# Kernel tuning notes

Measured on AMD Instinct MI355X. Metric: run time of the kernel, lower is better.

Reference implementation:

```python
import jax, jax.numpy as jnp
import numpy as np

B, X, H = 2048, 1024, 1024
DR = 0.5

def setup_inputs() -> dict:
    key = jax.random.key(0)
    ks = jax.random.split(key, 21)
    std = 1.0 / np.sqrt(H)
    u = lambda k, s: jax.random.uniform(k, s, jnp.float32, -std, std)
    bern = lambda k, s: (jax.random.bernoulli(k, 1.0 - DR, s) / (1.0 - DR)).astype(jnp.float32)
    return {
        "x": jax.random.normal(ks[0], (B, X), jnp.float32),
        "h0": jax.random.normal(ks[1], (B, H), jnp.float32),
        "c0": jax.random.normal(ks[2], (B, H), jnp.float32),
        "w_xi": u(ks[3], (H, X)), "w_xf": u(ks[4], (H, X)),
        "w_xc": u(ks[5], (H, X)), "w_xo": u(ks[6], (H, X)),
        "w_hi": u(ks[7], (H, H)), "w_hf": u(ks[8], (H, H)),
        "w_hc": u(ks[9], (H, H)), "w_ho": u(ks[10], (H, H)),
        "b_i": u(ks[11], (H,)), "b_f": u(ks[12], (H,)),
        "b_c": u(ks[13], (H,)), "b_o": u(ks[14], (H,)),
        "maskHI": bern(ks[15], (B, H)), "maskHF": bern(ks[16], (B, H)),
        "maskHC": bern(ks[17], (B, H)), "maskHO": bern(ks[18], (B, H)),
        "maskC": bern(ks[19], (B, H)),
    }

def reference(x, h0, c0,
              w_xi, w_xf, w_xc, w_xo,
              w_hi, w_hf, w_hc, w_ho,
              b_i, b_f, b_c, b_o,
              maskHI, maskHF, maskHC, maskHO, maskC):
    # gal dropout: per-gate masks on recurrent input h0
    hs = jnp.stack([h0 * maskHI, h0 * maskHF, h0 * maskHC, h0 * maskHO])  # [4,B,H]
    wh = jnp.stack([w_hi, w_hf, w_hc, w_ho])                              # [4,H,H]
    wx = jnp.stack([w_xi, w_xf, w_xc, w_xo])                              # [4,H,X]
    # two batched GEMMs (F.linear uses x @ W.T)
    g = jnp.einsum('bx,gkx->gbk', x, wx) + jnp.einsum('gbh,gkh->gbk', hs, wh)
    gateI = jax.nn.sigmoid(g[0] + b_i)
    gateF = jax.nn.sigmoid(g[1] + b_f)
    gateC = jnp.tanh(g[2] + b_c) * maskC   # sem dropout on candidate
    gateO = jax.nn.sigmoid(g[3] + b_o)
    c1 = gateF * c0 + gateI * gateC
    h1 = gateO * jnp.tanh(c1)
    return (h1, c1)
```

## Files before the change

### kernel.cpp

```cpp
#include <hip/hip_runtime.h>
#include <hip/hip_bf16.h>
#include <stdint.h>

#define BDIM 2048
#define HDIM 1024
#define XDIM 1024
#define BH (BDIM*HDIM)
#define WSEG 1048576

typedef __attribute__((ext_vector_type(8))) short short8;
typedef __attribute__((ext_vector_type(4))) float float4v;

__device__ __forceinline__ void gload16(const void* g, void* l) {
    __builtin_amdgcn_global_load_lds(
        (const __attribute__((address_space(1))) unsigned int*)g,
        (__attribute__((address_space(3))) unsigned int*)l, 16, 0, 0);
}

__device__ __forceinline__ unsigned pack2(float a, float b) {
    __hip_bfloat162 v = __float22bfloat162_rn(make_float2(a, b));
    return *reinterpret_cast<unsigned*>(&v);
}
__device__ __forceinline__ uint2 pack4(float4 f) {
    return make_uint2(pack2(f.x, f.y), pack2(f.z, f.w));
}

__global__ __launch_bounds__(256) void prep_all_k(
    const float* __restrict__ w0, const float* __restrict__ w1,
    const float* __restrict__ w2, const float* __restrict__ w3,
    const float* __restrict__ w4, const float* __restrict__ w5,
    const float* __restrict__ w6, const float* __restrict__ w7,
    const float* __restrict__ x, const float* __restrict__ h0,
    const float* __restrict__ mI, const float* __restrict__ mF,
    const float* __restrict__ mC, const float* __restrict__ mO,
    uint2* __restrict__ dst) {
    const int seg = blockIdx.y;
    const int i = blockIdx.x * 256 + threadIdx.x;
    float4 f;
    if (seg < 10) {
        const float* base;
        switch (seg) {
            case 0: base = w0; break; case 1: base = w1; break;
            case 2: base = w2; break; case 3: base = w3; break;
            case 4: base = w4; break; case 5: base = w5; break;
            case 6: base = w6; break; case 7: base = w7; break;
            default: base = x + (size_t)(seg - 8) * WSEG; break;
        }
        f = ((const float4*)base)[i];
    } else {
        const int s = seg - 10;
        const int g = s >> 1, half = s & 1;
        const float* mp = (g == 0) ? mI : (g == 1) ? mF : (g == 2) ? mC : mO;
        float4 h = ((const float4*)(h0 + (size_t)half * WSEG))[i];
        float4 m = ((const float4*)(mp + (size_t)half * WSEG))[i];
        f = make_float4(h.x * m.x, h.y * m.y, h.z * m.z, h.w * m.w);
    }
    dst[(size_t)seg * (WSEG / 4) + i] = pack4(f);
}

__global__ __launch_bounds__(256) void gemm_gates(
    const __hip_bfloat16* __restrict__ ws18,
    const float* __restrict__ bi, const float* __restrict__ bff,
    const float* __restrict__ bc, const float* __restrict__ bo,
    float* __restrict__ pre) {
    const int g = blockIdx.z;
    const __hip_bfloat16* wx = ws18 + (size_t)g * WSEG;
    const __hip_bfloat16* wh = ws18 + (size_t)(4 + g) * WSEG;
    const __hip_bfloat16* xb = ws18 + (size_t)8 * WSEG;
    const __hip_bfloat16* A2 = ws18 + (size_t)(10 + 2 * g) * WSEG;
    const float* bg = (g == 0) ? bi : (g == 1) ? bff : (g == 2) ? bc : bo;

    __shared__ __hip_bfloat16 As[128 * 32];
    __shared__ __hip_bfloat16 Bs[128 * 32];

    const int t = threadIdx.x;
    const int m0 = blockIdx.x * 128;
    const int n0 = blockIdx.y * 128;
    const int wv = t >> 6, lane = t & 63;
    const int wm = (wv >> 1) * 64, wn = (wv & 1) * 64;
    const int quad = lane >> 4, lrow = lane & 15;

    float4v acc[4][4];
#pragma unroll
    for (int i = 0; i < 4; ++i)
#pragma unroll
        for (int j = 0; j < 4; ++j) acc[i][j] = (float4v){0.f, 0.f, 0.f, 0.f};

    const short8* As8 = (const short8*)As;
    const short8* Bs8 = (const short8*)Bs;

#pragma unroll 1
    for (int half = 0; half < 2; ++half) {
        const __hip_bfloat16* Ap = half ? A2 : xb;
        const __hip_bfloat16* Bp = half ? wh : wx;
        for (int k0 = 0; k0 < 1024; k0 += 32) {
#pragma unroll
            for (int it = 0; it < 2; ++it) {
                int chunk = it * 256 + t;
                int row = chunk >> 2, cc = chunk & 3;
                gload16(Ap + (size_t)(m0 + row) * 1024 + k0 + cc * 8,
                        (char*)As + chunk * 16);
                gload16(Bp + (size_t)(n0 + row) * 1024 + k0 + cc * 8,
                        (char*)Bs + chunk * 16);
            }
            __syncthreads();

            short8 af[4], bfr[4];
#pragma unroll
            for (int mt = 0; mt < 4; ++mt) af[mt] = As8[(wm + mt * 16 + lrow) * 4 + quad];
#pragma unroll
            for (int nt = 0; nt < 4; ++nt) bfr[nt] = Bs8[(wn + nt * 16 + lrow) * 4 + quad];
#pragma unroll
            for (int mt = 0; mt < 4; ++mt)
#pragma unroll
                for (int nt = 0; nt < 4; ++nt)
                    acc[mt][nt] = __builtin_amdgcn_mfma_f32_16x16x32_bf16(
                        af[mt], bfr[nt], acc[mt][nt], 0, 0, 0);
            __syncthreads();
        }
    }

    float* preg = pre + (size_t)g * BH;
#pragma unroll
    for (int nt = 0; nt < 4; ++nt) {
        int col = n0 + wn + nt * 16 + lrow;
        float bias = bg[col];
#pragma unroll
        for (int mt = 0; mt < 4; ++mt) {
#pragma unroll
            for (int r = 0; r < 4; ++r) {
                int row = m0 + wm + mt * 16 + quad * 4 + r;
                preg[(size_t)row * HDIM + col] = acc[mt][nt][r] + bias;
            }
        }
    }
}

__global__ __launch_bounds__(256) void combine_k(
    const float* __restrict__ pre,
    const float* __restrict__ c0, const float* __restrict__ mC,
    float4* __restrict__ out) {
    const int i = blockIdx.x * 256 + threadIdx.x;
    float4 gi = ((const float4*)pre)[i];
    float4 gf = ((const float4*)(pre + BH))[i];
    float4 gc = ((const float4*)(pre + 2 * (size_t)BH))[i];
    float4 go = ((const float4*)(pre + 3 * (size_t)BH))[i];
    float4 vc0 = ((const float4*)c0)[i];
    float4 vmc = ((const float4*)mC)[i];

    float h1[4], c1[4];
#pragma unroll
    for (int j = 0; j < 4; ++j) {
        float xi = (j == 0) ? gi.x : (j == 1) ? gi.y : (j == 2) ? gi.z : gi.w;
        float xf = (j == 0) ? gf.x : (j == 1) ? gf.y : (j == 2) ? gf.z : gf.w;
        float xc = (j == 0) ? gc.x : (j == 1) ? gc.y : (j == 2) ? gc.z : gc.w;
        float xo = (j == 0) ? go.x : (j == 1) ? go.y : (j == 2) ? go.z : go.w;
        float cc0 = (j == 0) ? vc0.x : (j == 1) ? vc0.y : (j == 2) ? vc0.z : vc0.w;
        float mm = (j == 0) ? vmc.x : (j == 1) ? vmc.y : (j == 2) ? vmc.z : vmc.w;
        float I = 1.f / (1.f + __expf(-xi));
        float F = 1.f / (1.f + __expf(-xf));
        float C = tanhf(xc) * mm;
        float O = 1.f / (1.f + __expf(-xo));
        c1[j] = F * cc0 + I * C;
        h1[j] = O * tanhf(c1[j]);
    }
    out[i] = make_float4(h1[0], h1[1], h1[2], h1[3]);
    out[BH / 4 + i] = make_float4(c1[0], c1[1], c1[2], c1[3]);
}

extern "C" void kernel_launch(void* const* d_in, const int* in_sizes, int n_in,
                              void* d_out, int out_size, void* d_ws, size_t ws_size,
                              hipStream_t stream) {
    const float* x   = (const float*)d_in[0];
    const float* h0  = (const float*)d_in[1];
    const float* c0  = (const float*)d_in[2];
    const float* wxi = (const float*)d_in[3];
    const float* wxf = (const float*)d_in[4];
    const float* wxc = (const float*)d_in[5];
    const float* wxo = (const float*)d_in[6];
    const float* whi = (const float*)d_in[7];
    const float* whf = (const float*)d_in[8];
    const float* whc = (const float*)d_in[9];
    const float* who = (const float*)d_in[10];
    const float* bi  = (const float*)d_in[11];
    const float* bf  = (const float*)d_in[12];
    const float* bc  = (const float*)d_in[13];
    const float* bo  = (const float*)d_in[14];
    const float* mI  = (const float*)d_in[15];
    const float* mF  = (const float*)d_in[16];
    const float* mC  = (const float*)d_in[17];
    const float* mO  = (const float*)d_in[18];
    const float* mCell = (const float*)d_in[19];

    __hip_bfloat16* ws18 = (__hip_bfloat16*)d_ws;
    float* pre = (float*)(ws18 + (size_t)18 * WSEG);

    prep_all_k<<<dim3(WSEG / 4 / 256, 18), dim3(256), 0, stream>>>(
        wxi, wxf, wxc, wxo, whi, whf, whc, who, x, h0, mI, mF, mC, mO,
        (uint2*)ws18);

    gemm_gates<<<dim3(BDIM / 128, HDIM / 128, 4), dim3(256), 0, stream>>>(
        ws18, bi, bf, bc, bo, pre);

    combine_k<<<dim3(BH / 4 / 256), dim3(256), 0, stream>>>(
        pre, c0, mCell, (float4*)d_out);
}
```

Baseline: 215.5 us.

## Split-K gate GEMM into x/h halves with bf16 partials summed in combine

Splits each gate's GEMM into separate x-part and h-part blocks, doubling the grid to 1024 blocks and setting launch bounds for higher occupancy. Partial sums are written as bf16 and added together with the biases in the elementwise combine kernel. This aims to fill the GPU better and improve latency hiding; in exchange, each partial is rounded to bf16 before summation, which reduces accuracy.

```diff
diff --git a/kernel.cpp b/kernel.cpp
--- a/kernel.cpp
+++ b/kernel.cpp
@@ -23,6 +23,10 @@
 }
 __device__ __forceinline__ uint2 pack4(float4 f) {
     return make_uint2(pack2(f.x, f.y), pack2(f.z, f.w));
+}
+__device__ __forceinline__ float2 up2(unsigned u) {
+    __hip_bfloat162 v = *reinterpret_cast<__hip_bfloat162*>(&u);
+    return __bfloat1622float2(v);
 }
 
 __global__ __launch_bounds__(256) void prep_all_k(
@@ -58,17 +62,15 @@
     dst[(size_t)seg * (WSEG / 4) + i] = pack4(f);
 }
 
-__global__ __launch_bounds__(256) void gemm_gates(
+__global__ __launch_bounds__(256, 4) void gemm_split(
     const __hip_bfloat16* __restrict__ ws18,
-    const float* __restrict__ bi, const float* __restrict__ bff,
-    const float* __restrict__ bc, const float* __restrict__ bo,
-    float* __restrict__ pre) {
-    const int g = blockIdx.z;
-    const __hip_bfloat16* wx = ws18 + (size_t)g * WSEG;
-    const __hip_bfloat16* wh = ws18 + (size_t)(4 + g) * WSEG;
-    const __hip_bfloat16* xb = ws18 + (size_t)8 * WSEG;
-    const __hip_bfloat16* A2 = ws18 + (size_t)(10 + 2 * g) * WSEG;
-    const float* bg = (g == 0) ? bi : (g == 1) ? bff : (g == 2) ? bc : bo;
+    __hip_bfloat16* __restrict__ part) {
+    const int z = blockIdx.z;
+    const int g = z >> 1, half = z & 1;
+    const __hip_bfloat16* Ap = half ? (ws18 + (size_t)(10 + 2 * g) * WSEG)
+                                    : (ws18 + (size_t)8 * WSEG);
+    const __hip_bfloat16* Bp = half ? (ws18 + (size_t)(4 + g) * WSEG)
+                                    : (ws18 + (size_t)g * WSEG);
 
     __shared__ __hip_bfloat16 As[128 * 32];
     __shared__ __hip_bfloat16 Bs[128 * 32];
@@ -89,79 +91,93 @@
     const short8* As8 = (const short8*)As;
     const short8* Bs8 = (const short8*)Bs;
 
-#pragma unroll 1
-    for (int half = 0; half < 2; ++half) {
-        const __hip_bfloat16* Ap = half ? A2 : xb;
-        const __hip_bfloat16* Bp = half ? wh : wx;
-        for (int k0 = 0; k0 < 1024; k0 += 32) {
-#pragma unroll
-            for (int it = 0; it < 2; ++it) {
-                int chunk = it * 256 + t;
-                int row = chunk >> 2, cc = chunk & 3;
-                gload16(Ap + (size_t)(m0 + row) * 1024 + k0 + cc * 8,
-                        (char*)As + chunk * 16);
-                gload16(Bp + (size_t)(n0 + row) * 1024 + k0 + cc * 8,
-                        (char*)Bs + chunk * 16);
-            }
-            __syncthreads();
-
-            short8 af[4], bfr[4];
-#pragma unroll
-            for (int mt = 0; mt < 4; ++mt) af[mt] = As8[(wm + mt * 16 + lrow) * 4 + quad];
-#pragma unroll
-            for (int nt = 0; nt < 4; ++nt) bfr[nt] = Bs8[(wn + nt * 16 + lrow) * 4 + quad];
-#pragma unroll
-            for (int mt = 0; mt < 4; ++mt)
-#pragma unroll
-                for (int nt = 0; nt < 4; ++nt)
-                    acc[mt][nt] = __builtin_amdgcn_mfma_f32_16x16x32_bf16(
-                        af[mt], bfr[nt], acc[mt][nt], 0, 0, 0);
-            __syncthreads();
+    for (int k0 = 0; k0 < 1024; k0 += 32) {
+#pragma unroll
+        for (int it = 0; it < 2; ++it) {
+            int chunk = it * 256 + t;
+            int row = chunk >> 2, cc = chunk & 3;
+            gload16(Ap + (size_t)(m0 + row) * 1024 + k0 + cc * 8,
+                    (char*)As + chunk * 16);
+            gload16(Bp + (size_t)(n0 + row) * 1024 + k0 + cc * 8,
+                    (char*)Bs + chunk * 16);
         }
-    }
-
-    float* preg = pre + (size_t)g * BH;
+        __syncthreads();
+
+        short8 af[4], bfr[4];
+#pragma unroll
+        for (int mt = 0; mt < 4; ++mt) af[mt] = As8[(wm + mt * 16 + lrow) * 4 + quad];
+#pragma unroll
+        for (int nt = 0; nt < 4; ++nt) bfr[nt] = Bs8[(wn + nt * 16 + lrow) * 4 + quad];
+#pragma unroll
+        for (int mt = 0; mt < 4; ++mt)
+#pragma unroll
+            for (int nt = 0; nt < 4; ++nt)
+                acc[mt][nt] = __builtin_amdgcn_mfma_f32_16x16x32_bf16(
+                    af[mt], bfr[nt], acc[mt][nt], 0, 0, 0);
+        __syncthreads();
+    }
+
+    __hip_bfloat16* pz = part + (size_t)z * BH;
 #pragma unroll
     for (int nt = 0; nt < 4; ++nt) {
         int col = n0 + wn + nt * 16 + lrow;
-        float bias = bg[col];
 #pragma unroll
         for (int mt = 0; mt < 4; ++mt) {
 #pragma unroll
             for (int r = 0; r < 4; ++r) {
                 int row = m0 + wm + mt * 16 + quad * 4 + r;
-                preg[(size_t)row * HDIM + col] = acc[mt][nt][r] + bias;
+                pz[(size_t)row * HDIM + col] = __float2bfloat16(acc[mt][nt][r]);
             }
         }
     }
 }
 
 __global__ __launch_bounds__(256) void combine_k(
-    const float* __restrict__ pre,
+    const uint2* __restrict__ part,
+    const float* __restrict__ bi, const float* __restrict__ bff,
+    const float* __restrict__ bc, const float* __restrict__ bo,
     const float* __restrict__ c0, const float* __restrict__ mC,
     float4* __restrict__ out) {
     const int i = blockIdx.x * 256 + threadIdx.x;
-    float4 gi = ((const float4*)pre)[i];
-    float4 gf = ((const float4*)(pre + BH))[i];
-    float4 gc = ((const float4*)(pre + 2 * (size_t)BH))[i];
-    float4 go = ((const float4*)(pre + 3 * (size_t)BH))[i];
+    const int h4 = (i * 4 & (HDIM - 1)) >> 2;
+
+    float gate[4][4];
+#pragma unroll
+    for (int g = 0; g < 4; ++g) {
+        uint2 p0 = part[(size_t)(2 * g) * (BH / 4) + i];
+        uint2 p1 = part[(size_t)(2 * g + 1) * (BH / 4) + i];
+        float2 a0 = up2(p0.x), a1 = up2(p0.y);
+        float2 b0 = up2(p1.x), b1 = up2(p1.y);
+        gate[g][0] = a0.x + b0.x;
+        gate[g][1] = a0.y + b0.y;
+        gate[g][2] = a1.x + b1.x;
+        gate[g][3] = a1.y + b1.y;
+    }
+    float4 vbi = ((const float4*)bi)[h4];
+    float4 vbf = ((const float4*)bff)[h4];
+    float4 vbc = ((const float4*)bc)[h4];
+    float4 vbo = ((const float4*)bo)[h4];
     float4 vc0 = ((const float4*)c0)[i];
     float4 vmc = ((const float4*)mC)[i];
+    const float* pbi = (const float*)&vbi;
+    const float* pbf = (const float*)&vbf;
+    const float* pbc = (const float*)&vbc;
+    const float* pbo = (const float*)&vbo;
+    const float* pc0 = (const float*)&vc0;
+    const float* pmc = (const float*)&vmc;
 
     float h1[4], c1[4];
 #pragma unroll
     for (int j = 0; j < 4; ++j) {
-        float xi = (j == 0) ? gi.x : (j == 1) ? gi.y : (j == 2) ? gi.z : gi.w;
-        float xf = (j == 0) ? gf.x : (j == 1) ? gf.y : (j == 2) ? gf.z : gf.w;
-        float xc = (j == 0) ? gc.x : (j == 1) ? gc.y : (j == 2) ? gc.z : gc.w;
-        float xo = (j == 0) ? go.x : (j == 1) ? go.y : (j == 2) ? go.z : go.w;
-        float cc0 = (j == 0) ? vc0.x : (j == 1) ? vc0.y : (j == 2) ? vc0.z : vc0.w;
-        float mm = (j == 0) ? vmc.x : (j == 1) ? vmc.y : (j == 2) ? vmc.z : vmc.w;
+        float xi = gate[0][j] + pbi[j];
+        float xf = gate[1][j] + pbf[j];
+        float xc = gate[2][j] + pbc[j];
+        float xo = gate[3][j] + pbo[j];
         float I = 1.f / (1.f + __expf(-xi));
         float F = 1.f / (1.f + __expf(-xf));
-        float C = tanhf(xc) * mm;
+        float C = tanhf(xc) * pmc[j];
         float O = 1.f / (1.f + __expf(-xo));
-        c1[j] = F * cc0 + I * C;
+        c1[j] = F * pc0[j] + I * C;
         h1[j] = O * tanhf(c1[j]);
     }
     out[i] = make_float4(h1[0], h1[1], h1[2], h1[3]);
@@ -193,15 +209,15 @@
     const float* mCell = (const float*)d_in[19];
 
     __hip_bfloat16* ws18 = (__hip_bfloat16*)d_ws;
-    float* pre = (float*)(ws18 + (size_t)18 * WSEG);
+    __hip_bfloat16* part = ws18 + (size_t)18 * WSEG;
 
     prep_all_k<<<dim3(WSEG / 4 / 256, 18), dim3(256), 0, stream>>>(
         wxi, wxf, wxc, wxo, whi, whf, whc, who, x, h0, mI, mF, mC, mO,
         (uint2*)ws18);
 
-    gemm_gates<<<dim3(BDIM / 128, HDIM / 128, 4), dim3(256), 0, stream>>>(
-        ws18, bi, bf, bc, bo, pre);
+    gemm_split<<<dim3(BDIM / 128, HDIM / 128, 8), dim3(256), 0, stream>>>(
+        ws18, part);
 
     combine_k<<<dim3(BH / 4 / 256), dim3(256), 0, stream>>>(
-        pre, c0, mCell, (float4*)d_out);
-}
+        (const uint2*)part, bi, bf, bc, bo, c0, mCell, (float4*)d_out);
+}
```

New measurement: 213.9 us. About the same (-0.7%).
